# Optimization experiments

Hardware: AMD Instinct MI355X
Metric: run time of the kernel (lower is better)

The kernel has to match this reference:

```python
import jax, jax.numpy as jnp
import numpy as np

EMB = 768
HEADS = 8
HEAD_DIM = EMB // HEADS  # 96
SCALING = HEAD_DIM ** -0.5


def setup_inputs() -> dict:
    key = jax.random.key(0)
    ks = jax.random.split(key, 9)
    B, S = 2, 2048
    std = 1.0 / np.sqrt(EMB)
    x = jax.random.normal(ks[0], (B, S, EMB), dtype=jnp.float32)
    # torch nn.Linear weights are [out, in]; we store [in, out] for x @ W.
    Wq = jax.random.normal(ks[1], (EMB, EMB), dtype=jnp.float32) * std
    Wk = jax.random.normal(ks[2], (EMB, EMB), dtype=jnp.float32) * std
    Wv = jax.random.normal(ks[3], (EMB, EMB), dtype=jnp.float32) * std
    Wo = jax.random.normal(ks[4], (EMB, EMB), dtype=jnp.float32) * std
    bq = jax.random.normal(ks[5], (EMB,), dtype=jnp.float32) * std
    bk = jax.random.normal(ks[6], (EMB,), dtype=jnp.float32) * std
    bv = jax.random.normal(ks[7], (EMB,), dtype=jnp.float32) * std
    bo = jax.random.normal(ks[8], (EMB,), dtype=jnp.float32) * std
    return {"x": x, "Wq": Wq, "bq": bq, "Wk": Wk, "bk": bk,
            "Wv": Wv, "bv": bv, "Wo": Wo, "bo": bo}


def _split_heads(t):
    # [B, S, E] -> [B, H, S, D]
    B, S, _ = t.shape
    return t.reshape(B, S, HEADS, HEAD_DIM).transpose(0, 2, 1, 3)


def reference(x, Wq, bq, Wk, bk, Wv, bv, Wo, bo):
    q = _split_heads(x @ Wq + bq)
    k = _split_heads(x @ Wk + bk)
    v = _split_heads(x @ Wv + bv)
    # Full [B, H, S, S] score matrix, as in the source module.
    energies = jnp.einsum('bhqd,bhkd->bhqk', q, k)
    # Faithful quirk: softmax first, THEN multiply by scaling (dropout=0 -> identity).
    attention = jax.nn.softmax(energies, axis=-1) * SCALING
    out = jnp.einsum('bhqk,bhkd->bhqd', attention, v)
    B, H, S, D = out.shape
    out = out.transpose(0, 2, 1, 3).reshape(B, S, H * D)
    return out @ Wo + bo
```

## Files before the change

kernel.cpp:

```cpp
#include <hip/hip_runtime.h>
#include <hip/hip_bf16.h>

#define EMB 768
#define HD 96
#define NH 8
#define SEQ 2048
#define SCALING 0.10206207261596575f

typedef short bf16x8 __attribute__((ext_vector_type(8)));
typedef float f32x4  __attribute__((ext_vector_type(4)));
typedef unsigned short u16v8 __attribute__((ext_vector_type(8)));
typedef unsigned short u16v4 __attribute__((ext_vector_type(4)));

union F4 { float4 v; float f[4]; };

__device__ __forceinline__ unsigned short f2bf(float v) {
    __hip_bfloat16 b = __float2bfloat16(v);
    return *reinterpret_cast<unsigned short*>(&b);
}
__device__ __forceinline__ float bf2f(unsigned short u) {
    __hip_bfloat16 b = *reinterpret_cast<__hip_bfloat16*>(&u);
    return __bfloat162float(b);
}

__device__ __forceinline__ void dma16(const unsigned short* g, unsigned short* l) {
    __builtin_amdgcn_global_load_lds(
        (const __attribute__((address_space(1))) unsigned int*)g,
        (__attribute__((address_space(3))) unsigned int*)l,
        16, 0, 0);
}

__global__ __launch_bounds__(256) void convert_all(
    const float* __restrict__ x,
    const float* __restrict__ Wq, const float* __restrict__ Wk,
    const float* __restrict__ Wv, const float* __restrict__ Wo,
    unsigned short* __restrict__ xh, unsigned short* __restrict__ xl,
    unsigned short* __restrict__ WhT, unsigned short* __restrict__ WlT)
{
    __shared__ float T[64][68];
    if (blockIdx.x < 1536) {
        const size_t i0 = ((size_t)blockIdx.x * 256 + threadIdx.x) * 8;
        F4 a, b;
        a.v = *(const float4*)&x[i0];
        b.v = *(const float4*)&x[i0 + 4];
        u16v8 h, l;
        #pragma unroll
        for (int j = 0; j < 4; j++) {
            unsigned short hu = f2bf(a.f[j]);
            h[j] = hu; l[j] = f2bf(a.f[j] - bf2f(hu));
        }
        #pragma unroll
        for (int j = 0; j < 4; j++) {
            unsigned short hu = f2bf(b.f[j]);
            h[4+j] = hu; l[4+j] = f2bf(b.f[j] - bf2f(hu));
        }
        *(u16v8*)&xh[i0] = h;
        *(u16v8*)&xl[i0] = l;
    } else {
        const int tb = blockIdx.x - 1536;
        const int z  = tb / 144;
        const int r2 = tb - z*144;
        const int bx = r2 / 12, by = r2 - bx*12;
        const float* W = (z == 0) ? Wq : (z == 1) ? Wk : (z == 2) ? Wv : Wo;
        unsigned short* oh = WhT + (size_t)z * 589824;
        unsigned short* ol = WlT + (size_t)z * 589824;
        const int t = threadIdx.x;
        const int r = t >> 2, cg = (t & 3) * 16;
        const int k0 = bx * 64, n0 = by * 64;
        #pragma unroll
        for (int i = 0; i < 4; i++) {
            float4 v = *(const float4*)&W[(size_t)(k0 + r) * EMB + n0 + cg + 4*i];
            *(float4*)&T[r][cg + 4*i] = v;
        }
        __syncthreads();
        #pragma unroll
        for (int i = 0; i < 4; i++) {
            u16v4 h, l;
            #pragma unroll
            for (int j = 0; j < 4; j++) {
                float v = T[cg + 4*i + j][r];
                unsigned short hu = f2bf(v);
                h[j] = hu; l[j] = f2bf(v - bf2f(hu));
            }
            *(u16v4*)&oh[(size_t)(n0 + r) * EMB + k0 + cg + 4*i] = h;
            *(u16v4*)&ol[(size_t)(n0 + r) * EMB + k0 + cg + 4*i] = l;
        }
    }
}

#define QA_H 0
#define QA_L 4096
#define QW_H 8192
#define QW_L 12288

__global__ __launch_bounds__(256, 3) void qkv_mfma(
    const unsigned short* __restrict__ xh, const unsigned short* __restrict__ xl,
    const unsigned short* __restrict__ WhT, const unsigned short* __restrict__ WlT,
    const float* __restrict__ bq, const float* __restrict__ bk, const float* __restrict__ bv,
    unsigned short* __restrict__ Qh, unsigned short* __restrict__ Ql,
    unsigned short* __restrict__ Kb, unsigned short* __restrict__ Vt)
{
    const int which = blockIdx.z;
    const unsigned short* Wh = WhT + (size_t)which * 589824;
    const unsigned short* Wl = WlT + (size_t)which * 589824;
    const float* bias = (which == 0) ? bq : (which == 1) ? bk : bv;

    __shared__ __align__(16) unsigned short lds[16384];
    const int tid = threadIdx.x;
    const int lane = tid & 63, lo = lane & 15, h4 = lane >> 4;
    const int w = tid >> 6, wm = w & 1, wn = w >> 1;
    const int row0 = blockIdx.x * 128, col0 = blockIdx.y * 128;

    const unsigned short* sbase =
        (w == 0) ? xh + (size_t)row0 * EMB :
        (w == 1) ? xl + (size_t)row0 * EMB :
        (w == 2) ? Wh + (size_t)col0 * EMB :
                   Wl + (size_t)col0 * EMB;
    const int soff = w * 4096;

    f32x4 acc[4][4];
    #pragma unroll
    for (int i = 0; i < 4; i++)
        #pragma unroll
        for (int j = 0; j < 4; j++) acc[i][j] = (f32x4){0.f, 0.f, 0.f, 0.f};

    for (int k0 = 0; k0 < EMB; k0 += 32) {
        #pragma unroll
        for (int j = 0; j < 8; j++) {
            const int u = j*64 + lane;
            const int row = u >> 2, c8 = (u & 3) * 8;
            dma16(sbase + (size_t)row * EMB + k0 + c8, &lds[soff + j*512]);
        }
        __syncthreads();

        bf16x8 ah[4], al[4];
        #pragma unroll
        for (int i = 0; i < 4; i++)
            ah[i] = *(const bf16x8*)&lds[QA_H + (64*wm + 16*i + lo)*32 + 8*h4];
        if (which <= 1) {
            #pragma unroll
            for (int i = 0; i < 4; i++)
                al[i] = *(const bf16x8*)&lds[QA_L + (64*wm + 16*i + lo)*32 + 8*h4];
        }
        #pragma unroll
        for (int j = 0; j < 4; j++) {
            bf16x8 whf = *(const bf16x8*)&lds[QW_H + (64*wn + 16*j + lo)*32 + 8*h4];
            #pragma unroll
            for (int i = 0; i < 4; i++)
                acc[i][j] = __builtin_amdgcn_mfma_f32_16x16x32_bf16(ah[i], whf, acc[i][j], 0, 0, 0);
            if (which <= 1) {
                #pragma unroll
                for (int i = 0; i < 4; i++)
                    acc[i][j] = __builtin_amdgcn_mfma_f32_16x16x32_bf16(al[i], whf, acc[i][j], 0, 0, 0);
            }
            if (which != 1) {
                bf16x8 wlf = *(const bf16x8*)&lds[QW_L + (64*wn + 16*j + lo)*32 + 8*h4];
                #pragma unroll
                for (int i = 0; i < 4; i++)
                    acc[i][j] = __builtin_amdgcn_mfma_f32_16x16x32_bf16(ah[i], wlf, acc[i][j], 0, 0, 0);
            }
        }
        __syncthreads();
    }

    if (which == 0) {
        #pragma unroll
        for (int i = 0; i < 4; i++)
            #pragma unroll
            for (int r = 0; r < 4; r++) {
                const int sg = row0 + 64*wm + 16*i + 4*h4 + r;
                const int b = sg >> 11, s = sg & 2047;
                #pragma unroll
                for (int j = 0; j < 4; j++) {
                    const int c = col0 + 64*wn + 16*j + lo;
                    const int h = c / HD, d = c - h*HD;
                    float v = acc[i][j][r] + bias[c];
                    unsigned short hu = f2bf(v);
                    const size_t base = ((size_t)(b*NH + h) * SEQ + s) * HD + d;
                    Qh[base] = hu;
                    Ql[base] = f2bf(v - bf2f(hu));
                }
            }
    } else if (which == 1) {
        #pragma unroll
        for (int i = 0; i < 4; i++)
            #pragma unroll
            for (int r = 0; r < 4; r++) {
                const int sg = row0 + 64*wm + 16*i + 4*h4 + r;
                const int b = sg >> 11, s = sg & 2047;
                #pragma unroll
                for (int j = 0; j < 4; j++) {
                    const int c = col0 + 64*wn + 16*j + lo;
                    const int h = c / HD, d = c - h*HD;
                    float v = acc[i][j][r] + bias[c];
                    Kb[((size_t)(b*NH + h) * SEQ + s) * HD + d] = f2bf(v);
                }
            }
    } else {
        #pragma unroll
        for (int i = 0; i < 4; i++)
            #pragma unroll
            for (int r = 0; r < 4; r++) {
                const int sg = row0 + 64*wm + 16*i + 4*h4 + r;
                const int b = sg >> 11, s = sg & 2047;
                #pragma unroll
                for (int j = 0; j < 4; j++) {
                    const int c = col0 + 64*wn + 16*j + lo;
                    const int h = c / HD, d = c - h*HD;
                    float v = acc[i][j][r] + bias[c];
                    Vt[((size_t)(b*NH + h) * HD + d) * SEQ + s] = f2bf(v);
                }
            }
    }
}

#define PA_O 0
#define PWH_O 2048
#define PWL_O 4096

__global__ __launch_bounds__(256, 3) void proj_mfma(
    const unsigned short* __restrict__ AOh,
    const unsigned short* __restrict__ Wh, const unsigned short* __restrict__ Wl,
    const float* __restrict__ bo, float* __restrict__ out)
{
    __shared__ __align__(16) unsigned short lds[6144];
    const int tid = threadIdx.x;
    const int lane = tid & 63, lo = lane & 15, h4 = lane >> 4;
    const int w = tid >> 6, wm = w & 1, wn = w >> 1;
    const int row0 = blockIdx.x * 64, col0 = blockIdx.y * 64;
    const int r16 = lane >> 2, c8 = (lane & 3) * 8;

    f32x4 acc[2][2];
    #pragma unroll
    for (int i = 0; i < 2; i++)
        #pragma unroll
        for (int j = 0; j < 2; j++) acc[i][j] = (f32x4){0.f, 0.f, 0.f, 0.f};

    for (int k0 = 0; k0 < EMB; k0 += 32) {
        #pragma unroll
        for (int jj = 0; jj < 3; jj++) {
            const int u = w*3 + jj;
            const unsigned short* g; int ld;
            if (u < 4)      { g = AOh + (size_t)(row0 + u*16     + r16) * EMB + k0 + c8; ld = PA_O  + u*512; }
            else if (u < 8) { g = Wh  + (size_t)(col0 + (u-4)*16 + r16) * EMB + k0 + c8; ld = PWH_O + (u-4)*512; }
            else            { g = Wl  + (size_t)(col0 + (u-8)*16 + r16) * EMB + k0 + c8; ld = PWL_O + (u-8)*512; }
            dma16(g, &lds[ld]);
        }
        __syncthreads();

        bf16x8 af[2];
        #pragma unroll
        for (int i = 0; i < 2; i++)
            af[i] = *(const bf16x8*)&lds[PA_O + (32*wm + 16*i + lo)*32 + 8*h4];
        #pragma unroll
        for (int j = 0; j < 2; j++) {
            bf16x8 whf = *(const bf16x8*)&lds[PWH_O + (32*wn + 16*j + lo)*32 + 8*h4];
            bf16x8 wlf = *(const bf16x8*)&lds[PWL_O + (32*wn + 16*j + lo)*32 + 8*h4];
            #pragma unroll
            for (int i = 0; i < 2; i++) {
                acc[i][j] = __builtin_amdgcn_mfma_f32_16x16x32_bf16(af[i], whf, acc[i][j], 0, 0, 0);
                acc[i][j] = __builtin_amdgcn_mfma_f32_16x16x32_bf16(af[i], wlf, acc[i][j], 0, 0, 0);
            }
        }
        __syncthreads();
    }

    #pragma unroll
    for (int i = 0; i < 2; i++)
        #pragma unroll
        for (int r = 0; r < 4; r++) {
            const int sg = row0 + 32*wm + 16*i + 4*h4 + r;
            #pragma unroll
            for (int j = 0; j < 2; j++) {
                const int c = col0 + 32*wn + 16*j + lo;
                out[(size_t)sg * EMB + c] = acc[i][j][r] + bo[c];
            }
        }
}

#define ACH 13568
#define APAIR 27136
#define AP_OFF 54272

__global__ __launch_bounds__(512, 2) void attn_mfma(
    const unsigned short* __restrict__ Qh, const unsigned short* __restrict__ Ql,
    const unsigned short* __restrict__ Kb, const unsigned short* __restrict__ Vt,
    unsigned short* __restrict__ AOh)
{
    __shared__ __align__(16) unsigned short lds[72704];
    const int id   = blockIdx.x;
    const int xcd  = id & 7;
    const int j    = id >> 3;
    const int bh   = 2*xcd + (j & 1);
    const int q0   = (j >> 1) * 128;
    const int tid  = threadIdx.x;
    const int w    = tid >> 6;
    const int g    = w >> 2;
    const int wq   = w & 3;
    const int lane = tid & 63;
    const int lo   = lane & 15;
    const int h4   = lane >> 4;

    const unsigned short* KbH = Kb + (size_t)bh * SEQ * HD;
    const unsigned short* VtH = Vt + (size_t)bh * HD * SEQ;

    const unsigned short* sp0[6];
    int fK[6];
    int doff[6];
    #pragma unroll
    for (int r = 0; r < 6; r++) {
        const int e  = tid + 512*r;
        const int ch = (e >= 1536) ? 1 : 0;
        const int e2 = e - ch*1536;
        if (e2 < 768) {
            const int kk = e2 / 12, g8 = e2 - kk*12;
            sp0[r]  = KbH + (size_t)(ch*64 + kk) * HD + 8*g8;
            fK[r]   = HD;
            doff[r] = ch*ACH + kk*104 + 8*g8;
        } else {
            const int uv = e2 - 768, dV = uv >> 3, c8 = uv & 7;
            sp0[r]  = VtH + (size_t)dV*SEQ + ch*64 + 8*c8;
            fK[r]   = 1;
            doff[r] = ch*ACH + 6656 + dV*72 + 8*c8;
        }
    }

    bf16x8 qhf[2][3], qlf[2][3];
    #pragma unroll
    for (int mi = 0; mi < 2; mi++) {
        const size_t qoff = ((size_t)bh*SEQ + q0 + 32*wq + 16*mi + lo) * HD + 8*h4;
        #pragma unroll
        for (int ks = 0; ks < 3; ks++) {
            qhf[mi][ks] = *(const bf16x8*)&Qh[qoff + 32*ks];
            qlf[mi][ks] = *(const bf16x8*)&Ql[qoff + 32*ks];
        }
    }

    f32x4 O[2][6];
    #pragma unroll
    for (int mi = 0; mi < 2; mi++)
        #pragma unroll
        for (int i = 0; i < 6; i++) O[mi][i] = (f32x4){0.f, 0.f, 0.f, 0.f};
    float lsum[2][4] = {};

    unsigned short* Pw = lds + AP_OFF + w * 2304;

    #pragma unroll
    for (int r = 0; r < 6; r++)
        *(u16v8*)&lds[doff[r]] = *(const u16v8*)sp0[r];
    __syncthreads();

    #pragma unroll 1
    for (int u = 0; u < 16; u++) {
        const int kn0 = (u < 15) ? 128*(u + 1) : 0;
        u16v8 st[6];
        #pragma unroll
        for (int r = 0; r < 6; r++)
            st[r] = *(const u16v8*)(sp0[r] + (size_t)kn0 * fK[r]);

        const unsigned short* myK = lds + (u & 1)*APAIR + g*ACH;
        const unsigned short* myV = myK + 6656;

        f32x4 S[2][4];
        #pragma unroll
        for (int mi = 0; mi < 2; mi++)
            #pragma unroll
            for (int nb = 0; nb < 4; nb++) S[mi][nb] = (f32x4){0.f, 0.f, 0.f, 0.f};
        __builtin_amdgcn_s_setprio(1);
        #pragma unroll
        for (int ks = 0; ks < 3; ks++) {
            bf16x8 kf[4];
            #pragma unroll
            for (int nb = 0; nb < 4; nb++)
                kf[nb] = *(const bf16x8*)&myK[(16*nb + lo)*104 + 32*ks + 8*h4];
            #pragma unroll
            for (int nb = 0; nb < 4; nb++)
                #pragma unroll
                for (int mi = 0; mi < 2; mi++) {
                    S[mi][nb] = __builtin_amdgcn_mfma_f32_16x16x32_bf16(qhf[mi][ks], kf[nb], S[mi][nb], 0, 0, 0);
                    S[mi][nb] = __builtin_amdgcn_mfma_f32_16x16x32_bf16(qlf[mi][ks], kf[nb], S[mi][nb], 0, 0, 0);
                }
        }
        __builtin_amdgcn_s_setprio(0);

        #pragma unroll
        for (int mi = 0; mi < 2; mi++)
            #pragma unroll
            for (int nb = 0; nb < 4; nb++)
                #pragma unroll
                for (int r = 0; r < 4; r++) {
                    float p = __expf(S[mi][nb][r]);
                    lsum[mi][r] += p;
                    Pw[(16*mi + 4*h4 + r)*72 + 16*nb + lo] = f2bf(p);
                }

        __builtin_amdgcn_s_setprio(1);
        #pragma unroll
        for (int ks2 = 0; ks2 < 2; ks2++) {
            bf16x8 pf0 = *(const bf16x8*)&Pw[(lo)*72      + 32*ks2 + 8*h4];
            bf16x8 pf1 = *(const bf16x8*)&Pw[(16 + lo)*72 + 32*ks2 + 8*h4];
            #pragma unroll
            for (int nb2 = 0; nb2 < 6; nb2++) {
                bf16x8 vfv = *(const bf16x8*)&myV[(16*nb2 + lo)*72 + 32*ks2 + 8*h4];
                O[0][nb2] = __builtin_amdgcn_mfma_f32_16x16x32_bf16(pf0, vfv, O[0][nb2], 0, 0, 0);
                O[1][nb2] = __builtin_amdgcn_mfma_f32_16x16x32_bf16(pf1, vfv, O[1][nb2], 0, 0, 0);
            }
        }
        __builtin_amdgcn_s_setprio(0);

        unsigned short* dstp = lds + ((u + 1) & 1)*APAIR;
        #pragma unroll
        for (int r = 0; r < 6; r++)
            *(u16v8*)&dstp[doff[r]] = st[r];
        __syncthreads();
    }

    float* Fo = (float*)lds;
    float* Ls = (float*)lds + 12288;
    if (g == 1) {
        #pragma unroll
        for (int mi = 0; mi < 2; mi++)
            #pragma unroll
            for (int r = 0; r < 4; r++) {
                const int ql = 32*wq + 16*mi + 4*h4 + r;
                Ls[ql*16 + lo] = lsum[mi][r];
                #pragma unroll
                for (int nb2 = 0; nb2 < 6; nb2++)
                    Fo[ql*96 + 16*nb2 + lo] = O[mi][nb2][r];
            }
    }
    __syncthreads();
    if (g == 0) {
        const int b = bh >> 3, hh = bh & 7;
        #pragma unroll
        for (int mi = 0; mi < 2; mi++)
            #pragma unroll
            for (int r = 0; r < 4; r++) {
                const int ql = 32*wq + 16*mi + 4*h4 + r;
                float l = lsum[mi][r] + Ls[ql*16 + lo];
                l += __shfl_xor(l, 1);
                l += __shfl_xor(l, 2);
                l += __shfl_xor(l, 4);
                l += __shfl_xor(l, 8);
                const float sc = SCALING / l;
                const int q = q0 + ql;
                const size_t base = ((size_t)b*SEQ + q)*EMB + hh*HD + lo;
                #pragma unroll
                for (int nb2 = 0; nb2 < 6; nb2++)
                    AOh[base + 16*nb2] = f2bf((O[mi][nb2][r] + Fo[ql*96 + 16*nb2 + lo]) * sc);
            }
    }
}

extern "C" void kernel_launch(void* const* d_in, const int* in_sizes, int n_in,
                              void* d_out, int out_size, void* d_ws, size_t ws_size,
                              hipStream_t stream)
{
    const float* x  = (const float*)d_in[0];
    const float* Wq = (const float*)d_in[1];
    const float* bq = (const float*)d_in[2];
    const float* Wk = (const float*)d_in[3];
    const float* bk = (const float*)d_in[4];
    const float* Wv = (const float*)d_in[5];
    const float* bv = (const float*)d_in[6];
    const float* Wo = (const float*)d_in[7];
    const float* bo = (const float*)d_in[8];
    float* out = (float*)d_out;

    unsigned short* ws = (unsigned short*)d_ws;
    const size_t HS = (size_t)16 * SEQ * HD;
    const size_t WS1 = (size_t)EMB * EMB;
    unsigned short* Qh  = ws;
    unsigned short* Ql  = ws + HS;
    unsigned short* Kb  = ws + 2*HS;
    unsigned short* Vt  = ws + 3*HS;
    unsigned short* xh  = ws + 4*HS;
    unsigned short* xl  = ws + 5*HS;
    unsigned short* WhT = ws + 6*HS;
    unsigned short* WlT = ws + 6*HS + 4*WS1;
    unsigned short* AOh = xh;

    convert_all<<<2112, 256, 0, stream>>>(x, Wq, Wk, Wv, Wo, xh, xl, WhT, WlT);
    qkv_mfma<<<dim3(32, 6, 3), 256, 0, stream>>>(xh, xl, WhT, WlT, bq, bk, bv,
                                                 Qh, Ql, Kb, Vt);
    attn_mfma<<<256, 512, 0, stream>>>(Qh, Ql, Kb, Vt, AOh);
    proj_mfma<<<dim3(64, 12), 256, 0, stream>>>(AOh, WhT + 3*WS1, WlT + 3*WS1, bo, out);
}
```

Before: 204.1 us.

## Read K/V fragments directly from global memory instead of LDS staging

```diff
diff --git a/kernel.cpp b/kernel.cpp
--- a/kernel.cpp
+++ b/kernel.cpp
@@ -278,16 +278,12 @@
         }
 }
 
-#define ACH 13568
-#define APAIR 27136
-#define AP_OFF 54272
-
 __global__ __launch_bounds__(512, 2) void attn_mfma(
     const unsigned short* __restrict__ Qh, const unsigned short* __restrict__ Ql,
     const unsigned short* __restrict__ Kb, const unsigned short* __restrict__ Vt,
     unsigned short* __restrict__ AOh)
 {
-    __shared__ __align__(16) unsigned short lds[72704];
+    __shared__ __align__(16) unsigned short lds[28672];
     const int id   = blockIdx.x;
     const int xcd  = id & 7;
     const int j    = id >> 3;
@@ -304,27 +300,6 @@
     const unsigned short* KbH = Kb + (size_t)bh * SEQ * HD;
     const unsigned short* VtH = Vt + (size_t)bh * HD * SEQ;
 
-    const unsigned short* sp0[6];
-    int fK[6];
-    int doff[6];
-    #pragma unroll
-    for (int r = 0; r < 6; r++) {
-        const int e  = tid + 512*r;
-        const int ch = (e >= 1536) ? 1 : 0;
-        const int e2 = e - ch*1536;
-        if (e2 < 768) {
-            const int kk = e2 / 12, g8 = e2 - kk*12;
-            sp0[r]  = KbH + (size_t)(ch*64 + kk) * HD + 8*g8;
-            fK[r]   = HD;
-            doff[r] = ch*ACH + kk*104 + 8*g8;
-        } else {
-            const int uv = e2 - 768, dV = uv >> 3, c8 = uv & 7;
-            sp0[r]  = VtH + (size_t)dV*SEQ + ch*64 + 8*c8;
-            fK[r]   = 1;
-            doff[r] = ch*ACH + 6656 + dV*72 + 8*c8;
-        }
-    }
-
     bf16x8 qhf[2][3], qlf[2][3];
     #pragma unroll
     for (int mi = 0; mi < 2; mi++) {
@@ -343,23 +318,13 @@
         for (int i = 0; i < 6; i++) O[mi][i] = (f32x4){0.f, 0.f, 0.f, 0.f};
     float lsum[2][4] = {};
 
-    unsigned short* Pw = lds + AP_OFF + w * 2304;
-
-    #pragma unroll
-    for (int r = 0; r < 6; r++)
-        *(u16v8*)&lds[doff[r]] = *(const u16v8*)sp0[r];
-    __syncthreads();
+    unsigned short* Pw = lds + w * 2304;
 
     #pragma unroll 1
     for (int u = 0; u < 16; u++) {
-        const int kn0 = (u < 15) ? 128*(u + 1) : 0;
-        u16v8 st[6];
-        #pragma unroll
-        for (int r = 0; r < 6; r++)
-            st[r] = *(const u16v8*)(sp0[r] + (size_t)kn0 * fK[r]);
-
-        const unsigned short* myK = lds + (u & 1)*APAIR + g*ACH;
-        const unsigned short* myV = myK + 6656;
+        const int myc = 2*u + g;
+        const unsigned short* Kc = KbH + (size_t)myc * 64 * HD;
+        const unsigned short* Vc = VtH + (size_t)myc * 64;
 
         f32x4 S[2][4];
         #pragma unroll
@@ -372,7 +337,7 @@
             bf16x8 kf[4];
             #pragma unroll
             for (int nb = 0; nb < 4; nb++)
-                kf[nb] = *(const bf16x8*)&myK[(16*nb + lo)*104 + 32*ks + 8*h4];
+                kf[nb] = *(const bf16x8*)&Kc[(16*nb + lo)*HD + 32*ks + 8*h4];
             #pragma unroll
             for (int nb = 0; nb < 4; nb++)
                 #pragma unroll
@@ -401,19 +366,15 @@
             bf16x8 pf1 = *(const bf16x8*)&Pw[(16 + lo)*72 + 32*ks2 + 8*h4];
             #pragma unroll
             for (int nb2 = 0; nb2 < 6; nb2++) {
-                bf16x8 vfv = *(const bf16x8*)&myV[(16*nb2 + lo)*72 + 32*ks2 + 8*h4];
+                bf16x8 vfv = *(const bf16x8*)&Vc[(size_t)(16*nb2 + lo)*SEQ + 32*ks2 + 8*h4];
                 O[0][nb2] = __builtin_amdgcn_mfma_f32_16x16x32_bf16(pf0, vfv, O[0][nb2], 0, 0, 0);
                 O[1][nb2] = __builtin_amdgcn_mfma_f32_16x16x32_bf16(pf1, vfv, O[1][nb2], 0, 0, 0);
             }
         }
         __builtin_amdgcn_s_setprio(0);
-
-        unsigned short* dstp = lds + ((u + 1) & 1)*APAIR;
-        #pragma unroll
-        for (int r = 0; r < 6; r++)
-            *(u16v8*)&dstp[doff[r]] = st[r];
-        __syncthreads();
-    }
+    }
+
+    __syncthreads();
 
     float* Fo = (float*)lds;
     float* Ls = (float*)lds + 12288;
```

Result: slower. 253.1 us (+24.0%).
